# Optimization experiments

Measured on AMD Instinct MI355X. Metric: run time of the kernel, lower is better.

## Reference

```python
import jax, jax.numpy as jnp
import numpy as np

QLEN, MLEN, BSZ, D_MODEL, N_HEAD, D_HEAD = 1024, 1024, 4, 1024, 16, 64
KLEN = QLEN + MLEN
LN_EPS = 1e-5


def _linear(x, W, b):
    return x @ W + b


def _layer_norm(x, g, b):
    mu = jnp.mean(x, axis=-1, keepdims=True)
    var = jnp.var(x, axis=-1, keepdims=True)
    return (x - mu) * jax.lax.rsqrt(var + LN_EPS) * g + b


def _rel_shift(x):
    # x: [b, n, q, k] -> Transformer-XL rel-shift via zero-pad + reshape trick
    b, n, q, k = x.shape
    x = jnp.pad(x, ((0, 0), (0, 0), (0, 0), (1, 0)))
    x = x.reshape(b, n, k + 1, q)[:, :, 1:, :].reshape(b, n, q, k)
    return x


def setup_inputs() -> dict:
    key = jax.random.key(0)
    ks = jax.random.split(key, 16)
    s = 0.02
    inp = {
        "w": jax.random.normal(ks[0], (QLEN, BSZ, D_MODEL), jnp.float32),
        "r": jax.random.normal(ks[1], (KLEN, D_MODEL), jnp.float32),
        "r_w_bias": jax.random.normal(ks[2], (N_HEAD, D_HEAD), jnp.float32) * s,
        "r_r_bias": jax.random.normal(ks[3], (N_HEAD, D_HEAD), jnp.float32) * s,
        "mems": jax.random.normal(ks[4], (MLEN, BSZ, D_MODEL), jnp.float32),
        "Wq": jax.random.normal(ks[5], (D_MODEL, N_HEAD * D_HEAD), jnp.float32) * s,
        "bq": jnp.zeros((N_HEAD * D_HEAD,), jnp.float32),
        "Wk": jax.random.normal(ks[6], (D_MODEL, N_HEAD * D_HEAD), jnp.float32) * s,
        "bk": jnp.zeros((N_HEAD * D_HEAD,), jnp.float32),
        "Wv": jax.random.normal(ks[7], (D_MODEL, N_HEAD * D_HEAD), jnp.float32) * s,
        "bv": jnp.zeros((N_HEAD * D_HEAD,), jnp.float32),
        "Wr": jax.random.normal(ks[8], (D_MODEL, N_HEAD * D_HEAD), jnp.float32) * s,
        "br": jnp.zeros((N_HEAD * D_HEAD,), jnp.float32),
        "Wo": jax.random.normal(ks[9], (N_HEAD * D_HEAD, D_MODEL), jnp.float32) * s,
        "bo": jnp.zeros((D_MODEL,), jnp.float32),
        "ln_g": jnp.ones((D_MODEL,), jnp.float32),
        "ln_b": jnp.zeros((D_MODEL,), jnp.float32),
    }
    # causal mask with memory: key j visible to query i iff j <= i + MLEN
    inp["attn_mask"] = jnp.arange(KLEN)[None, :] > (jnp.arange(QLEN)[:, None] + MLEN)
    return inp


def reference(w, r, r_w_bias, r_r_bias, mems, Wq, bq, Wk, bk, Wv, bv, Wr, br,
              Wo, bo, ln_g, ln_b, attn_mask):
    qlen, bsz = w.shape[0], w.shape[1]
    scale = 1.0 / (D_HEAD ** 0.5)

    cat = jnp.concatenate([mems, w], axis=0)               # [klen, b, d]
    klen = cat.shape[0]

    q = _linear(cat, Wq, bq)[-qlen:]                       # [q, b, n*d]
    k = _linear(cat, Wk, bk)                               # [k, b, n*d]
    v = _linear(cat, Wv, bv)
    rk = _linear(r, Wr, br)                                # [rlen, n*d]

    q = q.reshape(qlen, bsz, N_HEAD, D_HEAD)
    k = k.reshape(klen, bsz, N_HEAD, D_HEAD)
    v = v.reshape(klen, bsz, N_HEAD, D_HEAD)
    rk = rk.reshape(r.shape[0], N_HEAD, D_HEAD)

    AC = jnp.einsum('ibnd,jbnd->bnij', q + r_w_bias, k)
    BD = jnp.einsum('ibnd,jnd->bnij', q + r_r_bias, rk)
    BD = _rel_shift(BD)

    attn_score = scale * (AC + BD)                          # [b, n, q, k]
    attn_score = jnp.where(attn_mask[None, None, :, :], -jnp.inf, attn_score)
    attn_prob = jax.nn.softmax(attn_score, axis=3)

    attn_vec = jnp.einsum('bnij,jbnd->ibnd', attn_prob, v)
    attn_vec = attn_vec.reshape(qlen, bsz, N_HEAD * D_HEAD)
    attn_out = _linear(attn_vec, Wo, bo)

    return _layer_norm(w + attn_out, ln_g, ln_b)            # post-lnorm path
```

## Files before the change

kernel.cpp:

```cpp
#include <hip/hip_runtime.h>
#include <stdint.h>


typedef unsigned short u16;
typedef unsigned int u32;
typedef __attribute__((ext_vector_type(8))) short s16x8;
typedef __attribute__((ext_vector_type(4))) float f32x4;

typedef const __attribute__((address_space(1))) void gvoid;
typedef __attribute__((address_space(3))) void lvoid;

__device__ __forceinline__ void async16(const u16* g, u16* l) {
  __builtin_amdgcn_global_load_lds((gvoid*)g, (lvoid*)l, 16, 0, 0);
}

__device__ __forceinline__ float b2f(u16 h) {
  union { u32 u; float f; } v; v.u = ((u32)h) << 16; return v.f;
}
__device__ __forceinline__ u16 f2b(float f) {
  union { float f; u32 u; } v; v.f = f; u32 u = v.u;
  return (u16)((u + 0x7FFFu + ((u >> 16) & 1u)) >> 16);
}
__device__ __forceinline__ bool is_bf16(const u16* lng) { return lng[0] == 0x3F80u; }

__device__ __forceinline__ void ld8(const void* p, size_t idx, bool bf, u16* dst) {
  if (bf) {
    *(uint4*)dst = *(const uint4*)((const u16*)p + idx);
  } else {
    const float* f = (const float*)p + idx;
    float4 a = *(const float4*)f;
    float4 c = *(const float4*)(f + 4);
    dst[0] = f2b(a.x); dst[1] = f2b(a.y); dst[2] = f2b(a.z); dst[3] = f2b(a.w);
    dst[4] = f2b(c.x); dst[5] = f2b(c.y); dst[6] = f2b(c.z); dst[7] = f2b(c.w);
  }
}
__device__ __forceinline__ float ldS(const void* p, int idx, bool bf) {
  return bf ? b2f(((const u16*)p)[idx]) : ((const float*)p)[idx];
}

__device__ __forceinline__ void gemm_bt_body(
    u16* As, u16* Bs,
    const void* Alo, const void* Ahi, int splitRow,
    const u16* BT, const void* bias,
    const void* eb0, const void* eb1,
    u16* C0, u16* C1, bool bfin, bool abf,
    int bm, int bnc)
{
  const int t = threadIdx.x;
  const int lane = t & 63, w = t >> 6;
  const int wr = w >> 1, wc = w & 1;
  const int ml = lane & 15, q = lane >> 4;

  f32x4 zero4 = {0.f, 0.f, 0.f, 0.f};
  f32x4 acc[4][4];
#pragma unroll
  for (int i = 0; i < 4; ++i)
#pragma unroll
    for (int j = 0; j < 4; ++j) acc[i][j] = zero4;

  const int srow = t >> 2;
  const int sch  = t & 3;
  const void* aptr[2]; size_t aidx[2]; const u16* bsrc[2];
#pragma unroll
  for (int p = 0; p < 2; ++p) {
    int gr = bm + srow + p * 64;
    if (gr < splitRow) { aptr[p] = Alo; aidx[p] = (size_t)gr * 1024 + sch * 8; }
    else { aptr[p] = Ahi; aidx[p] = (size_t)(gr - splitRow) * 1024 + sch * 8; }
    bsrc[p] = BT + (size_t)(bnc + srow + p * 64) * 1024 + sch * 8;
  }
  u16* lA[2] = { As + t * 8, As + 2048 + t * 8 };
  u16* lB[2] = { Bs + t * 8, Bs + 2048 + t * 8 };

  for (int kk = 0; kk < 1024; kk += 32) {
    if (abf) {
      __syncthreads();
      async16((const u16*)aptr[0] + aidx[0] + kk, lA[0]);
      async16((const u16*)aptr[1] + aidx[1] + kk, lA[1]);
      async16(bsrc[0] + kk, lB[0]);
      async16(bsrc[1] + kk, lB[1]);
      __syncthreads();
    } else {
      u16 ta0[8], ta1[8];
      ld8(aptr[0], aidx[0] + kk, false, ta0);
      ld8(aptr[1], aidx[1] + kk, false, ta1);
      uint4 vb0 = *(const uint4*)(bsrc[0] + kk);
      uint4 vb1 = *(const uint4*)(bsrc[1] + kk);
      __syncthreads();
      *(uint4*)lA[0] = *(uint4*)ta0;
      *(uint4*)lA[1] = *(uint4*)ta1;
      *(uint4*)lB[0] = vb0;
      *(uint4*)lB[1] = vb1;
      __syncthreads();
    }
    s16x8 af[4], bf[4];
#pragma unroll
    for (int mi = 0; mi < 4; ++mi)
      af[mi] = *(const s16x8*)&As[(wr * 64 + mi * 16 + ml) * 32 + q * 8];
#pragma unroll
    for (int ni = 0; ni < 4; ++ni)
      bf[ni] = *(const s16x8*)&Bs[(wc * 64 + ni * 16 + ml) * 32 + q * 8];
#pragma unroll
    for (int mi = 0; mi < 4; ++mi)
#pragma unroll
      for (int ni = 0; ni < 4; ++ni)
        acc[mi][ni] = __builtin_amdgcn_mfma_f32_16x16x32_bf16(af[mi], bf[ni],
                                                              acc[mi][ni], 0, 0, 0);
  }

#pragma unroll
  for (int ni = 0; ni < 4; ++ni) {
    int gcol = bnc + wc * 64 + ni * 16 + ml;
    float bi = ldS(bias, gcol, bfin);
    float e0 = eb0 ? ldS(eb0, gcol, bfin) : 0.f;
    float e1 = eb1 ? ldS(eb1, gcol, bfin) : 0.f;
#pragma unroll
    for (int mi = 0; mi < 4; ++mi)
#pragma unroll
      for (int rr = 0; rr < 4; ++rr) {
        int grow = bm + wr * 64 + mi * 16 + 4 * q + rr;
        size_t off = (size_t)grow * 1024 + gcol;
        float v0 = acc[mi][ni][rr] + bi;
        if (C1) { C0[off] = f2b(v0 + e0); C1[off] = f2b(v0 + e1); }
        else    { C0[off] = f2b(v0); }
      }
  }
}

__device__ __forceinline__ void gemm_vt_body(
    u16* As, u16* Bs,
    const void* Mlo, const void* Whi,
    const u16* WvT, const void* bv,
    u16* vT, bool bfin,
    int j0, int nc0, int b)
{
  const int t = threadIdx.x;
  const int lane = t & 63, w = t >> 6;
  const int wr = w >> 1, wc = w & 1;
  const int ml = lane & 15, q = lane >> 4;

  f32x4 zero4 = {0.f, 0.f, 0.f, 0.f};
  f32x4 acc[4][4];
#pragma unroll
  for (int i = 0; i < 4; ++i)
#pragma unroll
    for (int j = 0; j < 4; ++j) acc[i][j] = zero4;

  const int srow = t >> 2, sch = t & 3;
  const u16* asrc[2]; const void* bptr[2]; size_t bidx[2];
#pragma unroll
  for (int p = 0; p < 2; ++p) {
    asrc[p] = WvT + (size_t)(nc0 + srow + p * 64) * 1024 + sch * 8;
    int j = j0 + srow + p * 64;
    if (j < 1024) { bptr[p] = Mlo; bidx[p] = ((size_t)j * 4 + b) * 1024 + sch * 8; }
    else { bptr[p] = Whi; bidx[p] = ((size_t)(j - 1024) * 4 + b) * 1024 + sch * 8; }
  }
  u16* lA[2] = { As + t * 8, As + 2048 + t * 8 };
  u16* lB[2] = { Bs + t * 8, Bs + 2048 + t * 8 };

  for (int kk = 0; kk < 1024; kk += 32) {
    if (bfin) {
      __syncthreads();
      async16(asrc[0] + kk, lA[0]);
      async16(asrc[1] + kk, lA[1]);
      async16((const u16*)bptr[0] + bidx[0] + kk, lB[0]);
      async16((const u16*)bptr[1] + bidx[1] + kk, lB[1]);
      __syncthreads();
    } else {
      u16 tb0[8], tb1[8];
      ld8(bptr[0], bidx[0] + kk, false, tb0);
      ld8(bptr[1], bidx[1] + kk, false, tb1);
      __syncthreads();
      async16(asrc[0] + kk, lA[0]);
      async16(asrc[1] + kk, lA[1]);
      *(uint4*)lB[0] = *(uint4*)tb0;
      *(uint4*)lB[1] = *(uint4*)tb1;
      __syncthreads();
    }
    s16x8 af[4], bf[4];
#pragma unroll
    for (int mi = 0; mi < 4; ++mi)
      af[mi] = *(const s16x8*)&As[(wr * 64 + mi * 16 + ml) * 32 + q * 8];
#pragma unroll
    for (int ni = 0; ni < 4; ++ni)
      bf[ni] = *(const s16x8*)&Bs[(wc * 64 + ni * 16 + ml) * 32 + q * 8];
#pragma unroll
    for (int mi = 0; mi < 4; ++mi)
#pragma unroll
      for (int ni = 0; ni < 4; ++ni)
        acc[mi][ni] = __builtin_amdgcn_mfma_f32_16x16x32_bf16(af[mi], bf[ni],
                                                              acc[mi][ni], 0, 0, 0);
  }

#pragma unroll
  for (int mi = 0; mi < 4; ++mi)
#pragma unroll
    for (int rr = 0; rr < 4; ++rr) {
      int nc = nc0 + wr * 64 + mi * 16 + 4 * q + rr;
      float bi = ldS(bv, nc, bfin);
      size_t rbase = ((size_t)b * 1024 + nc) * 2048 + j0 + wc * 64 + ml * 4;
      u32 w0 = (u32)f2b(acc[mi][0][rr] + bi) | ((u32)f2b(acc[mi][1][rr] + bi) << 16);
      u32 w1 = (u32)f2b(acc[mi][2][rr] + bi) | ((u32)f2b(acc[mi][3][rr] + bi) << 16);
      uint2 pk; pk.x = w0; pk.y = w1;
      *(uint2*)(vT + rbase) = pk;
    }
}

__global__ __launch_bounds__(256) void gemm_bt(
    const void* __restrict__ Alo, const void* __restrict__ Ahi, int splitRow,
    const u16* __restrict__ BT, const void* __restrict__ bias,
    const void* __restrict__ eb0, const void* __restrict__ eb1,
    u16* __restrict__ C0, u16* __restrict__ C1,
    const u16* __restrict__ lng, int aIsInput)
{
  __shared__ u16 As[128 * 32];
  __shared__ u16 Bs[128 * 32];
  const bool bfin = is_bf16(lng);
  const bool abf = aIsInput ? bfin : true;
  gemm_bt_body(As, Bs, Alo, Ahi, splitRow, BT, bias, eb0, eb1, C0, C1,
               bfin, abf, blockIdx.y * 128, blockIdx.x * 128);
}

__global__ __launch_bounds__(256) void proj_uber(
    const void* __restrict__ mems, const void* __restrict__ w,
    const void* __restrict__ r,
    const u16* __restrict__ WkT, const void* __restrict__ bk,
    const u16* __restrict__ WvT, const void* __restrict__ bv,
    const u16* __restrict__ WqT, const void* __restrict__ bq,
    const void* __restrict__ rwb, const void* __restrict__ rrb,
    const u16* __restrict__ WrT, const void* __restrict__ br,
    u16* __restrict__ kb, u16* __restrict__ vT,
    u16* __restrict__ qw, u16* __restrict__ qr, u16* __restrict__ rkb,
    const u16* __restrict__ lng)
{
  __shared__ u16 As[128 * 32];
  __shared__ u16 Bs[128 * 32];
  const bool bfin = is_bf16(lng);
  int id = blockIdx.x;
  id = (id & 7) * 176 + (id >> 3);

  if (id < 512) {
    int bx = id & 7, by = id >> 3;
    gemm_bt_body(As, Bs, mems, w, 4096, WkT, bk, nullptr, nullptr,
                 kb, nullptr, bfin, bfin, by * 128, bx * 128);
  } else if (id < 1024) {
    int local = id - 512;
    int jx = local & 15, ny = (local >> 4) & 7, b = local >> 7;
    gemm_vt_body(As, Bs, mems, w, WvT, bv, vT, bfin, jx * 128, ny * 128, b);
  } else if (id < 1280) {
    int local = id - 1024;
    int bx = local & 7, by = local >> 3;
    gemm_bt_body(As, Bs, w, w, 4096, WqT, bq, rwb, rrb,
                 qw, qr, bfin, bfin, by * 128, bx * 128);
  } else {
    int local = id - 1280;
    int bx = local & 7, by = local >> 3;
    gemm_bt_body(As, Bs, r, r, 1 << 30, WrT, br, nullptr, nullptr,
                 rkb, nullptr, bfin, bfin, by * 128, bx * 128);
  }
}

__global__ __launch_bounds__(256) void transpose_w5(
    const void* __restrict__ W0, const void* __restrict__ W1,
    const void* __restrict__ W2, const void* __restrict__ W3,
    const void* __restrict__ W4,
    u16* __restrict__ T0, u16* __restrict__ T1, u16* __restrict__ T2,
    u16* __restrict__ T3, u16* __restrict__ T4, const u16* __restrict__ lng)
{
  __shared__ u16 tile[64 * 72];
  const bool bf = is_bf16(lng);
  const void* W; u16* T;
  switch (blockIdx.z) {
    case 0: W = W0; T = T0; break;
    case 1: W = W1; T = T1; break;
    case 2: W = W2; T = T2; break;
    case 3: W = W3; T = T3; break;
    default: W = W4; T = T4; break;
  }
  const int t = threadIdx.x;
  const int k0 = blockIdx.y * 64, n0 = blockIdx.x * 64;
#pragma unroll
  for (int p = 0; p < 2; ++p) {
    int s = p * 256 + t, row = s >> 3, ch = s & 7;
    u16 tmp[8];
    ld8(W, (size_t)(k0 + row) * 1024 + n0 + ch * 8, bf, tmp);
    *(uint4*)&tile[row * 72 + ch * 8] = *(uint4*)tmp;
  }
  __syncthreads();
#pragma unroll
  for (int p = 0; p < 2; ++p) {
    int s = p * 256 + t, nrow = s >> 3, ch = s & 7;
    union { u16 u[8]; uint4 v; } pk;
#pragma unroll
    for (int jj = 0; jj < 8; ++jj) pk.u[jj] = tile[(ch * 8 + jj) * 72 + nrow];
    *(uint4*)(T + (size_t)(n0 + nrow) * 1024 + k0 + ch * 8) = pk.v;
  }
}

__global__ __launch_bounds__(512, 4) void flash_attn(
    const u16* __restrict__ qw, const u16* __restrict__ qr,
    const u16* __restrict__ kb, const u16* __restrict__ vt,
    const u16* __restrict__ rkb, u16* __restrict__ av)
{
  constexpr int LP = 72;
  __shared__ u16 Ks[64 * LP];
  __shared__ u16 Vs[64 * LP];
  __shared__ u16 Rs[192 * LP];
  __shared__ u16 Ps[8][16 * LP];

  const int t = threadIdx.x;
  const int lane = t & 63, w = t >> 6;
  const int ml = lane & 15, q = lane >> 4;
  const int hbid = blockIdx.y * 8 + blockIdx.x;
  const int lbid = (hbid & 7) * 64 + (hbid >> 3);
  const int i0 = (lbid & 7) * 128;
  const int bn = lbid >> 3, b = bn >> 4, nh = bn & 15;

  s16x8 aqw[2], aqr[2];
  {
    size_t qo = ((size_t)(i0 + 16 * w + ml) * 4 + b) * 1024 + nh * 64 + q * 8;
    aqw[0] = *(const s16x8*)(qw + qo);
    aqw[1] = *(const s16x8*)(qw + qo + 32);
    aqr[0] = *(const s16x8*)(qr + qo);
    aqr[1] = *(const s16x8*)(qr + qo + 32);
  }

  f32x4 zero4 = {0.f, 0.f, 0.f, 0.f};
  f32x4 o[4];
#pragma unroll
  for (int dt = 0; dt < 4; ++dt) o[dt] = zero4;
  float lsum[4] = {0.f, 0.f, 0.f, 0.f};

  const int ntiles = min(i0 / 64 + 18, 32);
  const int c_lo = 16 * (7 - w);
  const int srow = t >> 3, sch = t & 7;

  uint4 pK, pV, pR;
  auto issue_kv = [&](int jt) {
    const int j0n = jt * 64;
    pK = *(const uint4*)(kb + ((size_t)(j0n + srow) * 4 + b) * 1024 + nh * 64 + sch * 8);
    pV = *(const uint4*)(vt + ((size_t)bn * 64 + srow) * 2048 + j0n + sch * 8);
  };
  auto rload = [&](int g) {
    g = g < 0 ? 0 : (g > 2047 ? 2047 : g);
    return *(const uint4*)(rkb + (size_t)g * 1024 + nh * 64 + sch * 8);
  };

  {
    issue_kv(0);
    uint4 r0 = rload(896 - i0 + srow);
    uint4 r1 = rload(896 - i0 + srow + 64);
    uint4 r2 = rload(896 - i0 + srow + 128);
    *(uint4*)&Ks[srow * LP + sch * 8] = pK;
    *(uint4*)&Vs[srow * LP + sch * 8] = pV;
    *(uint4*)&Rs[(srow      ) * LP + sch * 8] = r0;
    *(uint4*)&Rs[(srow +  64) * LP + sch * 8] = r1;
    *(uint4*)&Rs[(srow + 128) * LP + sch * 8] = r2;
  }
  __syncthreads();

  int slab = 0;
  int rbase = c_lo;
  for (int jt = 0; jt < ntiles; ++jt) {
    const int j0 = jt * 64;
    if (jt > 0) {
      __syncthreads();
      *(uint4*)&Ks[srow * LP + sch * 8] = pK;
      *(uint4*)&Vs[srow * LP + sch * 8] = pV;
      *(uint4*)&Rs[(slab * 64 + srow) * LP + sch * 8] = pR;
      slab = slab == 2 ? 0 : slab + 1;
      rbase += 64; if (rbase >= 192) rbase -= 192;
      __syncthreads();
    }
    if (jt + 1 < ntiles) {
      issue_kv(jt + 1);
      pR = rload(64 * jt + 1088 - i0 + srow);
    }

    f32x4 sac[4];
#pragma unroll
    for (int tt = 0; tt < 4; ++tt) sac[tt] = zero4;
#pragma unroll
    for (int ki = 0; ki < 2; ++ki)
#pragma unroll
      for (int tt = 0; tt < 4; ++tt) {
        s16x8 bfr = *(const s16x8*)&Ks[(tt * 16 + ml) * LP + ki * 32 + q * 8];
        sac[tt] = __builtin_amdgcn_mfma_f32_16x16x32_bf16(aqw[ki], bfr, sac[tt], 0, 0, 0);
      }

    f32x4 g[5];
#pragma unroll
    for (int ct = 0; ct < 5; ++ct) g[ct] = zero4;
#pragma unroll
    for (int ct = 0; ct < 5; ++ct) {
      int pb = rbase + ct * 16; if (pb >= 192) pb -= 192;
      const u16* rp = &Rs[(pb + ml) * LP + q * 8];
      s16x8 b0 = *(const s16x8*)(rp);
      s16x8 b1 = *(const s16x8*)(rp + 32);
      g[ct] = __builtin_amdgcn_mfma_f32_16x16x32_bf16(aqr[0], b0, g[ct], 0, 0, 0);
      g[ct] = __builtin_amdgcn_mfma_f32_16x16x32_bf16(aqr[1], b1, g[ct], 0, 0, 0);
    }

    const bool mtile = (j0 + 63) > (i0 + 1024);

#pragma unroll
    for (int rr = 0; rr < 4; ++rr) {
      const int r = 4 * q + rr;
      const int irow = i0 + 16 * w + r;
      const int L = ((ml - r + 15) & 15) | (q << 4);
      const bool hs = ml < 15 - r;
      float bl0 = hs ? g[1][rr] : g[0][rr];
      float bl1 = hs ? g[2][rr] : g[1][rr];
      float bl2 = hs ? g[3][rr] : g[2][rr];
      float bl3 = hs ? g[4][rr] : g[3][rr];
      float band0 = __shfl(bl0, L, 64);
      float band1 = __shfl(bl1, L, 64);
      float band2 = __shfl(bl2, L, 64);
      float band3 = __shfl(bl3, L, 64);
      float s0 = 0.125f * (sac[0][rr] + band0);
      float s1 = 0.125f * (sac[1][rr] + band1);
      float s2 = 0.125f * (sac[2][rr] + band2);
      float s3 = 0.125f * (sac[3][rr] + band3);
      if (mtile) {
        int lim = irow + 1024 - j0 - ml;
        if (0 > lim)  s0 = -3.0e38f;
        if (16 > lim) s1 = -3.0e38f;
        if (32 > lim) s2 = -3.0e38f;
        if (48 > lim) s3 = -3.0e38f;
      }
      float p0 = __expf(s0), p1 = __expf(s1), p2 = __expf(s2), p3 = __expf(s3);
      lsum[rr] += (p0 + p1) + (p2 + p3);
      u32 w0 = (u32)f2b(p0) | ((u32)f2b(p1) << 16);
      u32 w1 = (u32)f2b(p2) | ((u32)f2b(p3) << 16);
      uint2 pk; pk.x = w0; pk.y = w1;
      *(uint2*)&Ps[w][r * LP + ml * 4] = pk;
    }

#pragma unroll
    for (int ki = 0; ki < 2; ++ki) {
      s16x8 a = *(const s16x8*)&Ps[w][ml * LP + ki * 32 + q * 8];
#pragma unroll
      for (int dt = 0; dt < 4; ++dt) {
        s16x8 bfr = *(const s16x8*)&Vs[(dt * 16 + ml) * LP + ki * 32 + q * 8];
        o[dt] = __builtin_amdgcn_mfma_f32_16x16x32_bf16(a, bfr, o[dt], 0, 0, 0);
      }
    }
  }

#pragma unroll
  for (int rr = 0; rr < 4; ++rr) {
    float l = lsum[rr];
#pragma unroll
    for (int off = 1; off < 16; off <<= 1) l += __shfl_xor(l, off);
    float inv = 1.f / l;
    int i = i0 + 16 * w + 4 * q + rr;
#pragma unroll
    for (int dt = 0; dt < 4; ++dt)
      av[((size_t)i * 4 + b) * 1024 + nh * 64 + dt * 16 + ml] = f2b(o[dt][rr] * inv);
  }
}

__global__ __launch_bounds__(256) void ln_kernel(
    const void* __restrict__ wi, const u16* __restrict__ ao,
    const void* __restrict__ gg, const void* __restrict__ bb,
    void* __restrict__ out)
{
  __shared__ float red[8];
  const bool bf = is_bf16((const u16*)gg);
  const int t = threadIdx.x;
  const int row = blockIdx.x;
  const int base = row * 1024 + t * 4;
  float x0, x1, x2, x3;
  if (bf) {
    ushort4 xw = *(const ushort4*)((const u16*)wi + base);
    x0 = b2f(xw.x); x1 = b2f(xw.y); x2 = b2f(xw.z); x3 = b2f(xw.w);
  } else {
    float4 xw = *(const float4*)((const float*)wi + base);
    x0 = xw.x; x1 = xw.y; x2 = xw.z; x3 = xw.w;
  }
  ushort4 xa = *(const ushort4*)(ao + base);
  x0 += b2f(xa.x); x1 += b2f(xa.y); x2 += b2f(xa.z); x3 += b2f(xa.w);
  float s = x0 + x1 + x2 + x3;
  float s2 = x0 * x0 + x1 * x1 + x2 * x2 + x3 * x3;
#pragma unroll
  for (int off = 1; off < 64; off <<= 1) {
    s += __shfl_xor(s, off);
    s2 += __shfl_xor(s2, off);
  }
  if ((t & 63) == 0) { red[t >> 6] = s; red[4 + (t >> 6)] = s2; }
  __syncthreads();
  float S = red[0] + red[1] + red[2] + red[3];
  float S2 = red[4] + red[5] + red[6] + red[7];
  float mu = S * (1.f / 1024.f);
  float var = S2 * (1.f / 1024.f) - mu * mu;
  float inv = rsqrtf(var + 1e-5f);
  float g0 = ldS(gg, t * 4 + 0, bf), g1 = ldS(gg, t * 4 + 1, bf);
  float g2 = ldS(gg, t * 4 + 2, bf), g3 = ldS(gg, t * 4 + 3, bf);
  float b0 = ldS(bb, t * 4 + 0, bf), b1 = ldS(bb, t * 4 + 1, bf);
  float b2v = ldS(bb, t * 4 + 2, bf), b3 = ldS(bb, t * 4 + 3, bf);
  float y0 = (x0 - mu) * inv * g0 + b0;
  float y1 = (x1 - mu) * inv * g1 + b1;
  float y2 = (x2 - mu) * inv * g2 + b2v;
  float y3 = (x3 - mu) * inv * g3 + b3;
  if (bf) {
    ushort4 r;
    r.x = f2b(y0); r.y = f2b(y1); r.z = f2b(y2); r.w = f2b(y3);
    *(ushort4*)((u16*)out + base) = r;
  } else {
    float4 r; r.x = y0; r.y = y1; r.z = y2; r.w = y3;
    *(float4*)((float*)out + base) = r;
  }
}

__global__ __launch_bounds__(256) void copy_w(
    const void* __restrict__ wi, const u16* __restrict__ lng,
    void* __restrict__ out)
{
  const bool bf = is_bf16(lng);
  int i = blockIdx.x * 256 + threadIdx.x;
  if (bf) ((u16*)out)[i] = ((const u16*)wi)[i];
  else    ((float*)out)[i] = ((const float*)wi)[i];
}

extern "C" void kernel_launch(void* const* d_in, const int* in_sizes, int n_in,
                              void* d_out, int out_size, void* d_ws, size_t ws_size,
                              hipStream_t stream) {
  (void)in_sizes; (void)n_in; (void)out_size;
  const void* w    = d_in[0];
  const void* r    = d_in[1];
  const void* rwb  = d_in[2];
  const void* rrb  = d_in[3];
  const void* mems = d_in[4];
  const void* Wq   = d_in[5];
  const void* bq   = d_in[6];
  const void* Wk   = d_in[7];
  const void* bk   = d_in[8];
  const void* Wv   = d_in[9];
  const void* bv   = d_in[10];
  const void* Wr   = d_in[11];
  const void* br   = d_in[12];
  const void* Wo   = d_in[13];
  const void* bo   = d_in[14];
  const u16*  lng  = (const u16*)d_in[15];
  const void* lnb  = d_in[16];

  dim3 blk(256);
  const size_t M = (size_t)1 << 20;
  const size_t NEED = 31 * M * 2;
  if (ws_size < NEED) {
    copy_w<<<dim3(16384), blk, 0, stream>>>(w, lng, d_out);
    return;
  }

  u16* ws  = (u16*)d_ws;
  u16* WqT = ws + 0 * M;
  u16* WkT = ws + 1 * M;
  u16* WvT = ws + 2 * M;
  u16* WrT = ws + 3 * M;
  u16* WoT = ws + 4 * M;
  u16* kb  = ws + 5 * M;
  u16* vT  = ws + 13 * M;
  u16* qw  = ws + 21 * M;
  u16* qr  = ws + 25 * M;
  u16* rkb = ws + 29 * M;
  u16* av  = ws + 0 * M;
  u16* ao  = qw;

  transpose_w5<<<dim3(16, 16, 5), blk, 0, stream>>>(Wq, Wk, Wv, Wr, Wo,
                                                    WqT, WkT, WvT, WrT, WoT, lng);
  proj_uber<<<dim3(1408), blk, 0, stream>>>(mems, w, r,
                                            WkT, bk, WvT, bv, WqT, bq, rwb, rrb,
                                            WrT, br, kb, vT, qw, qr, rkb, lng);
  flash_attn<<<dim3(8, 64), dim3(512), 0, stream>>>(qw, qr, kb, vT, rkb, av);
  gemm_bt<<<dim3(8, 32), blk, 0, stream>>>(av, av, 1 << 30, WoT, bo,
                                           nullptr, nullptr, ao, nullptr, lng, 0);
  ln_kernel<<<dim3(4096), blk, 0, stream>>>(w, ao, lng, lnb, d_out);
}
```

Baseline: 368.5 us.

## Double-buffer GEMM LDS staging and balance flash-attention query-block order

Converts the bf16 async GEMM paths (gemm_bt_body and gemm_vt_body) to a two-buffer LDS pipeline. The next K-slice is issued into the alternate buffer while MFMAs run on the current one, which drops one barrier per iteration and overlaps global loads with compute. LDS per block doubles to 32 KB, which may reduce occupancy. Flash attention also remaps the query-block index so half the block groups run in reverse order, meant to interleave long and short causal tiles across CUs.

Measured after the change: 369.7 us. No clear change (+0.3%).

```diff
diff --git a/kernel.cpp b/kernel.cpp
--- a/kernel.cpp
+++ b/kernel.cpp
@@ -68,43 +68,67 @@
     else { aptr[p] = Ahi; aidx[p] = (size_t)(gr - splitRow) * 1024 + sch * 8; }
     bsrc[p] = BT + (size_t)(bnc + srow + p * 64) * 1024 + sch * 8;
   }
-  u16* lA[2] = { As + t * 8, As + 2048 + t * 8 };
-  u16* lB[2] = { Bs + t * 8, Bs + 2048 + t * 8 };
-
-  for (int kk = 0; kk < 1024; kk += 32) {
-    if (abf) {
-      __syncthreads();
-      async16((const u16*)aptr[0] + aidx[0] + kk, lA[0]);
-      async16((const u16*)aptr[1] + aidx[1] + kk, lA[1]);
-      async16(bsrc[0] + kk, lB[0]);
-      async16(bsrc[1] + kk, lB[1]);
-      __syncthreads();
-    } else {
+
+  if (abf) {
+    auto stage = [&](int buf, int kk) {
+      u16* a = As + buf * 4096 + t * 8;
+      u16* b = Bs + buf * 4096 + t * 8;
+      async16((const u16*)aptr[0] + aidx[0] + kk, a);
+      async16((const u16*)aptr[1] + aidx[1] + kk, a + 2048);
+      async16(bsrc[0] + kk, b);
+      async16(bsrc[1] + kk, b + 2048);
+    };
+    stage(0, 0);
+    __syncthreads();
+    int cur = 0;
+    for (int kk = 0; kk < 1024; kk += 32) {
+      if (kk + 32 < 1024) stage(cur ^ 1, kk + 32);
+      const u16* Ab = As + cur * 4096;
+      const u16* Bb = Bs + cur * 4096;
+      s16x8 af[4], bf[4];
+#pragma unroll
+      for (int mi = 0; mi < 4; ++mi)
+        af[mi] = *(const s16x8*)&Ab[(wr * 64 + mi * 16 + ml) * 32 + q * 8];
+#pragma unroll
+      for (int ni = 0; ni < 4; ++ni)
+        bf[ni] = *(const s16x8*)&Bb[(wc * 64 + ni * 16 + ml) * 32 + q * 8];
+#pragma unroll
+      for (int mi = 0; mi < 4; ++mi)
+#pragma unroll
+        for (int ni = 0; ni < 4; ++ni)
+          acc[mi][ni] = __builtin_amdgcn_mfma_f32_16x16x32_bf16(af[mi], bf[ni],
+                                                                acc[mi][ni], 0, 0, 0);
+      __syncthreads();
+      cur ^= 1;
+    }
+  } else {
+    for (int kk = 0; kk < 1024; kk += 32) {
       u16 ta0[8], ta1[8];
       ld8(aptr[0], aidx[0] + kk, false, ta0);
       ld8(aptr[1], aidx[1] + kk, false, ta1);
       uint4 vb0 = *(const uint4*)(bsrc[0] + kk);
       uint4 vb1 = *(const uint4*)(bsrc[1] + kk);
       __syncthreads();
-      *(uint4*)lA[0] = *(uint4*)ta0;
-      *(uint4*)lA[1] = *(uint4*)ta1;
-      *(uint4*)lB[0] = vb0;
-      *(uint4*)lB[1] = vb1;
-      __syncthreads();
-    }
-    s16x8 af[4], bf[4];
-#pragma unroll
-    for (int mi = 0; mi < 4; ++mi)
-      af[mi] = *(const s16x8*)&As[(wr * 64 + mi * 16 + ml) * 32 + q * 8];
-#pragma unroll
-    for (int ni = 0; ni < 4; ++ni)
-      bf[ni] = *(const s16x8*)&Bs[(wc * 64 + ni * 16 + ml) * 32 + q * 8];
-#pragma unroll
-    for (int mi = 0; mi < 4; ++mi)
+      *(uint4*)(As + t * 8) = *(uint4*)ta0;
+      *(uint4*)(As + 2048 + t * 8) = *(uint4*)ta1;
+      *(uint4*)(Bs + t * 8) = vb0;
+      *(uint4*)(Bs + 2048 + t * 8) = vb1;
+      __syncthreads();
+      s16x8 af[4], bf[4];
+#pragma unroll
+      for (int mi = 0; mi < 4; ++mi)
+        af[mi] = *(const s16x8*)&As[(wr * 64 + mi * 16 + ml) * 32 + q * 8];
 #pragma unroll
       for (int ni = 0; ni < 4; ++ni)
-        acc[mi][ni] = __builtin_amdgcn_mfma_f32_16x16x32_bf16(af[mi], bf[ni],
-                                                              acc[mi][ni], 0, 0, 0);
+        bf[ni] = *(const s16x8*)&Bs[(wc * 64 + ni * 16 + ml) * 32 + q * 8];
+#pragma unroll
+      for (int mi = 0; mi < 4; ++mi)
+#pragma unroll
+        for (int ni = 0; ni < 4; ++ni)
+          acc[mi][ni] = __builtin_amdgcn_mfma_f32_16x16x32_bf16(af[mi], bf[ni],
+                                                                acc[mi][ni], 0, 0, 0);
+      __syncthreads();
+    }
   }
 
 #pragma unroll
@@ -154,41 +178,65 @@
     if (j < 1024) { bptr[p] = Mlo; bidx[p] = ((size_t)j * 4 + b) * 1024 + sch * 8; }
     else { bptr[p] = Whi; bidx[p] = ((size_t)(j - 1024) * 4 + b) * 1024 + sch * 8; }
   }
-  u16* lA[2] = { As + t * 8, As + 2048 + t * 8 };
-  u16* lB[2] = { Bs + t * 8, Bs + 2048 + t * 8 };
-
-  for (int kk = 0; kk < 1024; kk += 32) {
-    if (bfin) {
-      __syncthreads();
-      async16(asrc[0] + kk, lA[0]);
-      async16(asrc[1] + kk, lA[1]);
-      async16((const u16*)bptr[0] + bidx[0] + kk, lB[0]);
-      async16((const u16*)bptr[1] + bidx[1] + kk, lB[1]);
-      __syncthreads();
-    } else {
+
+  if (bfin) {
+    auto stage = [&](int buf, int kk) {
+      u16* a = As + buf * 4096 + t * 8;
+      u16* b2 = Bs + buf * 4096 + t * 8;
+      async16(asrc[0] + kk, a);
+      async16(asrc[1] + kk, a + 2048);
+      async16((const u16*)bptr[0] + bidx[0] + kk, b2);
+      async16((const u16*)bptr[1] + bidx[1] + kk, b2 + 2048);
+    };
+    stage(0, 0);
+    __syncthreads();
+    int cur = 0;
+    for (int kk = 0; kk < 1024; kk += 32) {
+      if (kk + 32 < 1024) stage(cur ^ 1, kk + 32);
+      const u16* Ab = As + cur * 4096;
+      const u16* Bb = Bs + cur * 4096;
+      s16x8 af[4], bf[4];
+#pragma unroll
+      for (int mi = 0; mi < 4; ++mi)
+        af[mi] = *(const s16x8*)&Ab[(wr * 64 + mi * 16 + ml) * 32 + q * 8];
+#pragma unroll
+      for (int ni = 0; ni < 4; ++ni)
+        bf[ni] = *(const s16x8*)&Bb[(wc * 64 + ni * 16 + ml) * 32 + q * 8];
+#pragma unroll
+      for (int mi = 0; mi < 4; ++mi)
+#pragma unroll
+        for (int ni = 0; ni < 4; ++ni)
+          acc[mi][ni] = __builtin_amdgcn_mfma_f32_16x16x32_bf16(af[mi], bf[ni],
+                                                                acc[mi][ni], 0, 0, 0);
+      __syncthreads();
+      cur ^= 1;
+    }
+  } else {
+    for (int kk = 0; kk < 1024; kk += 32) {
       u16 tb0[8], tb1[8];
       ld8(bptr[0], bidx[0] + kk, false, tb0);
       ld8(bptr[1], bidx[1] + kk, false, tb1);
       __syncthreads();
-      async16(asrc[0] + kk, lA[0]);
-      async16(asrc[1] + kk, lA[1]);
-      *(uint4*)lB[0] = *(uint4*)tb0;
-      *(uint4*)lB[1] = *(uint4*)tb1;
-      __syncthreads();
-    }
-    s16x8 af[4], bf[4];
-#pragma unroll
-    for (int mi = 0; mi < 4; ++mi)
-      af[mi] = *(const s16x8*)&As[(wr * 64 + mi * 16 + ml) * 32 + q * 8];
-#pragma unroll
-    for (int ni = 0; ni < 4; ++ni)
-      bf[ni] = *(const s16x8*)&Bs[(wc * 64 + ni * 16 + ml) * 32 + q * 8];
-#pragma unroll
-    for (int mi = 0; mi < 4; ++mi)
+      async16(asrc[0] + kk, As + t * 8);
+      async16(asrc[1] + kk, As + 2048 + t * 8);
+      *(uint4*)(Bs + t * 8) = *(uint4*)tb0;
+      *(uint4*)(Bs + 2048 + t * 8) = *(uint4*)tb1;
+      __syncthreads();
+      s16x8 af[4], bf[4];
+#pragma unroll
+      for (int mi = 0; mi < 4; ++mi)
+        af[mi] = *(const s16x8*)&As[(wr * 64 + mi * 16 + ml) * 32 + q * 8];
 #pragma unroll
       for (int ni = 0; ni < 4; ++ni)
-        acc[mi][ni] = __builtin_amdgcn_mfma_f32_16x16x32_bf16(af[mi], bf[ni],
-                                                              acc[mi][ni], 0, 0, 0);
+        bf[ni] = *(const s16x8*)&Bs[(wc * 64 + ni * 16 + ml) * 32 + q * 8];
+#pragma unroll
+      for (int mi = 0; mi < 4; ++mi)
+#pragma unroll
+        for (int ni = 0; ni < 4; ++ni)
+          acc[mi][ni] = __builtin_amdgcn_mfma_f32_16x16x32_bf16(af[mi], bf[ni],
+                                                                acc[mi][ni], 0, 0, 0);
+      __syncthreads();
+    }
   }
 
 #pragma unroll
@@ -212,8 +260,8 @@
     u16* __restrict__ C0, u16* __restrict__ C1,
     const u16* __restrict__ lng, int aIsInput)
 {
-  __shared__ u16 As[128 * 32];
-  __shared__ u16 Bs[128 * 32];
+  __shared__ u16 As[2 * 4096];
+  __shared__ u16 Bs[2 * 4096];
   const bool bfin = is_bf16(lng);
   const bool abf = aIsInput ? bfin : true;
   gemm_bt_body(As, Bs, Alo, Ahi, splitRow, BT, bias, eb0, eb1, C0, C1,
@@ -232,8 +280,8 @@
     u16* __restrict__ qw, u16* __restrict__ qr, u16* __restrict__ rkb,
     const u16* __restrict__ lng)
 {
-  __shared__ u16 As[128 * 32];
-  __shared__ u16 Bs[128 * 32];
+  __shared__ u16 As[2 * 4096];
+  __shared__ u16 Bs[2 * 4096];
   const bool bfin = is_bf16(lng);
   int id = blockIdx.x;
   id = (id & 7) * 176 + (id >> 3);
@@ -312,7 +360,9 @@
   const int ml = lane & 15, q = lane >> 4;
   const int hbid = blockIdx.y * 8 + blockIdx.x;
   const int lbid = (hbid & 7) * 64 + (hbid >> 3);
-  const int i0 = (lbid & 7) * 128;
+  const int L = lbid & 63;
+  const int i0idx = (L < 32) ? (L & 7) : 7 - (L & 7);
+  const int i0 = i0idx * 128;
   const int bn = lbid >> 3, b = bn >> 4, nh = bn & 15;
 
   s16x8 aqw[2], aqr[2];
@@ -406,16 +456,16 @@
     for (int rr = 0; rr < 4; ++rr) {
       const int r = 4 * q + rr;
       const int irow = i0 + 16 * w + r;
-      const int L = ((ml - r + 15) & 15) | (q << 4);
+      const int L2 = ((ml - r + 15) & 15) | (q << 4);
       const bool hs = ml < 15 - r;
       float bl0 = hs ? g[1][rr] : g[0][rr];
       float bl1 = hs ? g[2][rr] : g[1][rr];
       float bl2 = hs ? g[3][rr] : g[2][rr];
       float bl3 = hs ? g[4][rr] : g[3][rr];
-      float band0 = __shfl(bl0, L, 64);
-      float band1 = __shfl(bl1, L, 64);
-      float band2 = __shfl(bl2, L, 64);
-      float band3 = __shfl(bl3, L, 64);
+      float band0 = __shfl(bl0, L2, 64);
+      float band1 = __shfl(bl1, L2, 64);
+      float band2 = __shfl(bl2, L2, 64);
+      float band3 = __shfl(bl3, L2, 64);
       float s0 = 0.125f * (sac[0][rr] + band0);
       float s1 = 0.125f * (sac[1][rr] + band1);
       float s2 = 0.125f * (sac[2][rr] + band2);
```

## Widen GEMM K-tile to 64 with XOR-swizzled LDS and balance flash-attn tile order

Applied to the files above, without the earlier changes.

The projection GEMMs (gemm_bt and the V-transpose GEMM) now stage a 64-wide K slice per iteration instead of 32. LDS is laid out with an XOR swizzle on the 16-byte chunk index, which is meant to avoid bank conflicts on the fragment reads. This halves the number of barrier pairs per K loop and doubles the MFMA work between syncs, at the cost of twice the shared memory per block. Flash attention also remaps query-tile indices so that consecutive blocks alternate ascending and descending causal lengths, to balance work across CUs.

Result: slower. 403.9 us (+9.6%).

```diff
diff --git a/kernel.cpp b/kernel.cpp
--- a/kernel.cpp
+++ b/kernel.cpp
@@ -58,53 +58,61 @@
 #pragma unroll
     for (int j = 0; j < 4; ++j) acc[i][j] = zero4;
 
-  const int srow = t >> 2;
-  const int sch  = t & 3;
-  const void* aptr[2]; size_t aidx[2]; const u16* bsrc[2];
-#pragma unroll
-  for (int p = 0; p < 2; ++p) {
-    int gr = bm + srow + p * 64;
-    if (gr < splitRow) { aptr[p] = Alo; aidx[p] = (size_t)gr * 1024 + sch * 8; }
-    else { aptr[p] = Ahi; aidx[p] = (size_t)(gr - splitRow) * 1024 + sch * 8; }
-    bsrc[p] = BT + (size_t)(bnc + srow + p * 64) * 1024 + sch * 8;
-  }
-  u16* lA[2] = { As + t * 8, As + 2048 + t * 8 };
-  u16* lB[2] = { Bs + t * 8, Bs + 2048 + t * 8 };
-
-  for (int kk = 0; kk < 1024; kk += 32) {
+  const int srow = t >> 3;
+  const int scol = (((t & 7) ^ ((t >> 3) & 7)) << 3);
+  const void* aptr[4]; size_t aidx[4]; const u16* bsrc[4];
+#pragma unroll
+  for (int p = 0; p < 4; ++p) {
+    int gr = bm + p * 32 + srow;
+    if (gr < splitRow) { aptr[p] = Alo; aidx[p] = (size_t)gr * 1024 + scol; }
+    else { aptr[p] = Ahi; aidx[p] = (size_t)(gr - splitRow) * 1024 + scol; }
+    bsrc[p] = BT + (size_t)(bnc + p * 32 + srow) * 1024 + scol;
+  }
+
+  for (int kk = 0; kk < 1024; kk += 64) {
     if (abf) {
       __syncthreads();
-      async16((const u16*)aptr[0] + aidx[0] + kk, lA[0]);
-      async16((const u16*)aptr[1] + aidx[1] + kk, lA[1]);
-      async16(bsrc[0] + kk, lB[0]);
-      async16(bsrc[1] + kk, lB[1]);
+#pragma unroll
+      for (int p = 0; p < 4; ++p) {
+        async16((const u16*)aptr[p] + aidx[p] + kk, As + p * 2048 + t * 8);
+        async16(bsrc[p] + kk, Bs + p * 2048 + t * 8);
+      }
       __syncthreads();
     } else {
-      u16 ta0[8], ta1[8];
-      ld8(aptr[0], aidx[0] + kk, false, ta0);
-      ld8(aptr[1], aidx[1] + kk, false, ta1);
-      uint4 vb0 = *(const uint4*)(bsrc[0] + kk);
-      uint4 vb1 = *(const uint4*)(bsrc[1] + kk);
-      __syncthreads();
-      *(uint4*)lA[0] = *(uint4*)ta0;
-      *(uint4*)lA[1] = *(uint4*)ta1;
-      *(uint4*)lB[0] = vb0;
-      *(uint4*)lB[1] = vb1;
-      __syncthreads();
-    }
-    s16x8 af[4], bf[4];
-#pragma unroll
-    for (int mi = 0; mi < 4; ++mi)
-      af[mi] = *(const s16x8*)&As[(wr * 64 + mi * 16 + ml) * 32 + q * 8];
-#pragma unroll
-    for (int ni = 0; ni < 4; ++ni)
-      bf[ni] = *(const s16x8*)&Bs[(wc * 64 + ni * 16 + ml) * 32 + q * 8];
-#pragma unroll
-    for (int mi = 0; mi < 4; ++mi)
-#pragma unroll
-      for (int ni = 0; ni < 4; ++ni)
-        acc[mi][ni] = __builtin_amdgcn_mfma_f32_16x16x32_bf16(af[mi], bf[ni],
-                                                              acc[mi][ni], 0, 0, 0);
+      u16 ta[4][8]; uint4 tb[4];
+#pragma unroll
+      for (int p = 0; p < 4; ++p) {
+        ld8(aptr[p], aidx[p] + kk, false, ta[p]);
+        tb[p] = *(const uint4*)(bsrc[p] + kk);
+      }
+      __syncthreads();
+#pragma unroll
+      for (int p = 0; p < 4; ++p) {
+        *(uint4*)(As + p * 2048 + t * 8) = *(uint4*)ta[p];
+        *(uint4*)(Bs + p * 2048 + t * 8) = tb[p];
+      }
+      __syncthreads();
+    }
+#pragma unroll
+    for (int ki = 0; ki < 2; ++ki) {
+      s16x8 af[4], bf[4];
+#pragma unroll
+      for (int mi = 0; mi < 4; ++mi) {
+        int row = wr * 64 + mi * 16 + ml;
+        af[mi] = *(const s16x8*)&As[row * 64 + ((((ki << 2) + q) ^ (ml & 7)) << 3)];
+      }
+#pragma unroll
+      for (int ni = 0; ni < 4; ++ni) {
+        int row = wc * 64 + ni * 16 + ml;
+        bf[ni] = *(const s16x8*)&Bs[row * 64 + ((((ki << 2) + q) ^ (ml & 7)) << 3)];
+      }
+#pragma unroll
+      for (int mi = 0; mi < 4; ++mi)
+#pragma unroll
+        for (int ni = 0; ni < 4; ++ni)
+          acc[mi][ni] = __builtin_amdgcn_mfma_f32_16x16x32_bf16(af[mi], bf[ni],
+                                                                acc[mi][ni], 0, 0, 0);
+    }
   }
 
 #pragma unroll
@@ -145,50 +153,58 @@
 #pragma unroll
     for (int j = 0; j < 4; ++j) acc[i][j] = zero4;
 
-  const int srow = t >> 2, sch = t & 3;
-  const u16* asrc[2]; const void* bptr[2]; size_t bidx[2];
-#pragma unroll
-  for (int p = 0; p < 2; ++p) {
-    asrc[p] = WvT + (size_t)(nc0 + srow + p * 64) * 1024 + sch * 8;
-    int j = j0 + srow + p * 64;
-    if (j < 1024) { bptr[p] = Mlo; bidx[p] = ((size_t)j * 4 + b) * 1024 + sch * 8; }
-    else { bptr[p] = Whi; bidx[p] = ((size_t)(j - 1024) * 4 + b) * 1024 + sch * 8; }
-  }
-  u16* lA[2] = { As + t * 8, As + 2048 + t * 8 };
-  u16* lB[2] = { Bs + t * 8, Bs + 2048 + t * 8 };
-
-  for (int kk = 0; kk < 1024; kk += 32) {
+  const int srow = t >> 3;
+  const int scol = (((t & 7) ^ ((t >> 3) & 7)) << 3);
+  const u16* asrc[4]; const void* bptr[4]; size_t bidx[4];
+#pragma unroll
+  for (int p = 0; p < 4; ++p) {
+    asrc[p] = WvT + (size_t)(nc0 + p * 32 + srow) * 1024 + scol;
+    int j = j0 + p * 32 + srow;
+    if (j < 1024) { bptr[p] = Mlo; bidx[p] = ((size_t)j * 4 + b) * 1024 + scol; }
+    else { bptr[p] = Whi; bidx[p] = ((size_t)(j - 1024) * 4 + b) * 1024 + scol; }
+  }
+
+  for (int kk = 0; kk < 1024; kk += 64) {
     if (bfin) {
       __syncthreads();
-      async16(asrc[0] + kk, lA[0]);
-      async16(asrc[1] + kk, lA[1]);
-      async16((const u16*)bptr[0] + bidx[0] + kk, lB[0]);
-      async16((const u16*)bptr[1] + bidx[1] + kk, lB[1]);
+#pragma unroll
+      for (int p = 0; p < 4; ++p) {
+        async16(asrc[p] + kk, As + p * 2048 + t * 8);
+        async16((const u16*)bptr[p] + bidx[p] + kk, Bs + p * 2048 + t * 8);
+      }
       __syncthreads();
     } else {
-      u16 tb0[8], tb1[8];
-      ld8(bptr[0], bidx[0] + kk, false, tb0);
-      ld8(bptr[1], bidx[1] + kk, false, tb1);
-      __syncthreads();
-      async16(asrc[0] + kk, lA[0]);
-      async16(asrc[1] + kk, lA[1]);
-      *(uint4*)lB[0] = *(uint4*)tb0;
-      *(uint4*)lB[1] = *(uint4*)tb1;
-      __syncthreads();
-    }
-    s16x8 af[4], bf[4];
-#pragma unroll
-    for (int mi = 0; mi < 4; ++mi)
-      af[mi] = *(const s16x8*)&As[(wr * 64 + mi * 16 + ml) * 32 + q * 8];
-#pragma unroll
-    for (int ni = 0; ni < 4; ++ni)
-      bf[ni] = *(const s16x8*)&Bs[(wc * 64 + ni * 16 + ml) * 32 + q * 8];
-#pragma unroll
-    for (int mi = 0; mi < 4; ++mi)
-#pragma unroll
-      for (int ni = 0; ni < 4; ++ni)
-        acc[mi][ni] = __builtin_amdgcn_mfma_f32_16x16x32_bf16(af[mi], bf[ni],
-                                                              acc[mi][ni], 0, 0, 0);
+      u16 tb[4][8];
+#pragma unroll
+      for (int p = 0; p < 4; ++p) ld8(bptr[p], bidx[p] + kk, false, tb[p]);
+      __syncthreads();
+#pragma unroll
+      for (int p = 0; p < 4; ++p) {
+        async16(asrc[p] + kk, As + p * 2048 + t * 8);
+        *(uint4*)(Bs + p * 2048 + t * 8) = *(uint4*)tb[p];
+      }
+      __syncthreads();
+    }
+#pragma unroll
+    for (int ki = 0; ki < 2; ++ki) {
+      s16x8 af[4], bf[4];
+#pragma unroll
+      for (int mi = 0; mi < 4; ++mi) {
+        int row = wr * 64 + mi * 16 + ml;
+        af[mi] = *(const s16x8*)&As[row * 64 + ((((ki << 2) + q) ^ (ml & 7)) << 3)];
+      }
+#pragma unroll
+      for (int ni = 0; ni < 4; ++ni) {
+        int row = wc * 64 + ni * 16 + ml;
+        bf[ni] = *(const s16x8*)&Bs[row * 64 + ((((ki << 2) + q) ^ (ml & 7)) << 3)];
+      }
+#pragma unroll
+      for (int mi = 0; mi < 4; ++mi)
+#pragma unroll
+        for (int ni = 0; ni < 4; ++ni)
+          acc[mi][ni] = __builtin_amdgcn_mfma_f32_16x16x32_bf16(af[mi], bf[ni],
+                                                                acc[mi][ni], 0, 0, 0);
+    }
   }
 
 #pragma unroll
@@ -212,8 +228,8 @@
     u16* __restrict__ C0, u16* __restrict__ C1,
     const u16* __restrict__ lng, int aIsInput)
 {
-  __shared__ u16 As[128 * 32];
-  __shared__ u16 Bs[128 * 32];
+  __shared__ u16 As[128 * 64];
+  __shared__ u16 Bs[128 * 64];
   const bool bfin = is_bf16(lng);
   const bool abf = aIsInput ? bfin : true;
   gemm_bt_body(As, Bs, Alo, Ahi, splitRow, BT, bias, eb0, eb1, C0, C1,
@@ -232,8 +248,8 @@
     u16* __restrict__ qw, u16* __restrict__ qr, u16* __restrict__ rkb,
     const u16* __restrict__ lng)
 {
-  __shared__ u16 As[128 * 32];
-  __shared__ u16 Bs[128 * 32];
+  __shared__ u16 As[128 * 64];
+  __shared__ u16 Bs[128 * 64];
   const bool bfin = is_bf16(lng);
   int id = blockIdx.x;
   id = (id & 7) * 176 + (id >> 3);
@@ -312,7 +328,9 @@
   const int ml = lane & 15, q = lane >> 4;
   const int hbid = blockIdx.y * 8 + blockIdx.x;
   const int lbid = (hbid & 7) * 64 + (hbid >> 3);
-  const int i0 = (lbid & 7) * 128;
+  const int L = lbid & 63;
+  const int i0idx = (L < 32) ? (L & 7) : 7 - (L & 7);
+  const int i0 = i0idx * 128;
   const int bn = lbid >> 3, b = bn >> 4, nh = bn & 15;
 
   s16x8 aqw[2], aqr[2];
@@ -406,16 +424,16 @@
     for (int rr = 0; rr < 4; ++rr) {
       const int r = 4 * q + rr;
       const int irow = i0 + 16 * w + r;
-      const int L = ((ml - r + 15) & 15) | (q << 4);
+      const int L2 = ((ml - r + 15) & 15) | (q << 4);
       const bool hs = ml < 15 - r;
       float bl0 = hs ? g[1][rr] : g[0][rr];
       float bl1 = hs ? g[2][rr] : g[1][rr];
       float bl2 = hs ? g[3][rr] : g[2][rr];
       float bl3 = hs ? g[4][rr] : g[3][rr];
-      float band0 = __shfl(bl0, L, 64);
-      float band1 = __shfl(bl1, L, 64);
-      float band2 = __shfl(bl2, L, 64);
-      float band3 = __shfl(bl3, L, 64);
+      float band0 = __shfl(bl0, L2, 64);
+      float band1 = __shfl(bl1, L2, 64);
+      float band2 = __shfl(bl2, L2, 64);
+      float band3 = __shfl(bl3, L2, 64);
       float s0 = 0.125f * (sac[0][rr] + band0);
       float s1 = 0.125f * (sac[1][rr] + band1);
       float s2 = 0.125f * (sac[2][rr] + band2);
```
